# Optimization experiments

Measured on AMD Instinct MI355X. Metric: run time of the kernel, lower is better.

## Reference

```python
import jax, jax.numpy as jnp
import numpy as np

QMIN, QMAX = -128.0, 127.0  # 8-bit signed activation range


def fq_act(x, s):
    """Fake-quantize activations: clip(round(x/s))*s with straight-through estimator."""
    y = jnp.clip(jnp.round(x / s), QMIN, QMAX) * s
    return x + jax.lax.stop_gradient(y - x)


def fq_weight(w):
    """Per-tensor max-abs symmetric (narrow-range) 8-bit weight fake-quant with STE."""
    s = jnp.max(jnp.abs(w)) / 127.0
    y = jnp.clip(jnp.round(w / s), -127.0, 127.0) * s
    return w + jax.lax.stop_gradient(y - w)


def conv1x1(x, w, b):
    # x: [b,c,h,w], w: [o,c] -> [b,o,h,w]
    return jnp.einsum('bchw,oc->bohw', x, w) + b[None, :, None, None]


def setup_inputs() -> dict:
    key = jax.random.key(0)
    ks = jax.random.split(key, 6)
    B, C, HC, H, W = 8, 64, 32, 64, 64
    x = jax.random.normal(ks[0], (B, C, H, W), dtype=jnp.float32)
    wq = jax.random.normal(ks[1], (HC, C), dtype=jnp.float32) * 0.05
    wk = jax.random.normal(ks[2], (HC, C), dtype=jnp.float32) * 0.05
    wv = jax.random.normal(ks[3], (HC, C), dtype=jnp.float32) * 0.05
    wp = jax.random.normal(ks[4], (C, HC), dtype=jnp.float32) * 0.05
    return {
        'x': x,
        'wq': wq, 'bq': jnp.zeros((HC,), jnp.float32),
        'wk': wk, 'bk': jnp.zeros((HC,), jnp.float32),
        'wv': wv, 'bv': jnp.zeros((HC,), jnp.float32),
        'wp': wp, 'bp': jnp.zeros((C,), jnp.float32),
        's_in': jnp.ones((1,), jnp.float32) * 0.0625,
        's_out': jnp.ones((1,), jnp.float32) * 0.0625,
    }


def reference(x, wq, bq, wk, bk, wv, bv, wp, bp, s_in, s_out):
    b, c, h, w = x.shape
    hc = wq.shape[0]
    n = h * w
    xq = fq_act(x, s_in)                              # quant_inp(x)
    q = conv1x1(xq, fq_weight(wq), bq).reshape(b, hc, n).transpose(0, 2, 1)  # [b,n,hc]
    k = conv1x1(xq, fq_weight(wk), bk).reshape(b, hc, n)                     # [b,hc,n]
    v = conv1x1(xq, fq_weight(wv), bv).reshape(b, hc, n).transpose(0, 2, 1)  # [b,n,hc]
    z = jax.nn.softmax(jnp.einsum('bqc,bck->bqk', q, k), axis=-1)            # [b,n,n]
    z = jnp.einsum('bqk,bkc->bqc', z, v).transpose(0, 2, 1).reshape(b, hc, h, w)
    z = fq_act(z, s_in)                               # quant_inp(z) (shared module/scale)
    out = xq + conv1x1(z, fq_weight(wp), bp)
    return fq_act(out, s_out)                         # self.act QuantIdentity
```

## Files before the change

### kernel.cpp

```cpp
#include <hip/hip_runtime.h>
#include <hip/hip_bf16.h>
#include <cstdint>
#include <cstddef>

#define NB 8
#define NC 64
#define NHC 32
#define NN 4096
#define LOG2E 1.44269504088896340736f

typedef short v8s __attribute__((ext_vector_type(8)));
typedef float v4f __attribute__((ext_vector_type(4)));
typedef unsigned int v4u __attribute__((ext_vector_type(4)));

__device__ __forceinline__ unsigned short f2b(float f) {
    unsigned int u = __builtin_bit_cast(unsigned int, f);
    u += 0x7fffu + ((u >> 16) & 1u);
    return (unsigned short)(u >> 16);
}
__device__ __forceinline__ float b2f(unsigned short s) {
    unsigned int u = ((unsigned int)s) << 16;
    return __builtin_bit_cast(float, u);
}
__device__ __forceinline__ unsigned int pack2_bf16(float a, float b) {
    unsigned int ua = __builtin_bit_cast(unsigned int, a);
    ua += 0x7fffu + ((ua >> 16) & 1u);
    unsigned int ub = __builtin_bit_cast(unsigned int, b);
    ub += 0x7fffu + ((ub >> 16) & 1u);
    return (ua >> 16) | (ub & 0xffff0000u);
}
__device__ __forceinline__ unsigned int trunc2_bf16(float a, float b) {
    return __builtin_amdgcn_perm(__builtin_bit_cast(unsigned int, b),
                                 __builtin_bit_cast(unsigned int, a), 0x07060302u);
}
__device__ __forceinline__ float wave_max(float v) {
    #pragma unroll
    for (int off = 1; off < 64; off <<= 1) v = fmaxf(v, __shfl_xor(v, off));
    return v;
}

__global__ __launch_bounds__(256) void k_qkv(
    const float* __restrict__ x,
    const float* __restrict__ wq, const float* __restrict__ wk, const float* __restrict__ wv,
    const float* __restrict__ bq, const float* __restrict__ bk, const float* __restrict__ bv,
    const float* __restrict__ s_in,
    unsigned short* __restrict__ xqb, unsigned short* __restrict__ qb,
    unsigned short* __restrict__ kb, unsigned short* __restrict__ vb)
{
    int blk = blockIdx.x;
    int b   = blk & 7;
    int seg = blk >> 3;
    int p0  = seg * 64;
    int tid = threadIdx.x;
    int wave = tid >> 6;
    int lane = tid & 63;

    __shared__ __align__(16) unsigned short xt[64][72];
    __shared__ __align__(16) unsigned short wlds[6144];
    __shared__ float red[3][4];

    float4 q0 = *(const float4*)(wq + tid * 8), q1 = *(const float4*)(wq + tid * 8 + 4);
    float4 k0 = *(const float4*)(wk + tid * 8), k1 = *(const float4*)(wk + tid * 8 + 4);
    float4 v0 = *(const float4*)(wv + tid * 8), v1 = *(const float4*)(wv + tid * 8 + 4);
    float mq = fmaxf(fmaxf(fmaxf(fabsf(q0.x), fabsf(q0.y)), fmaxf(fabsf(q0.z), fabsf(q0.w))),
                     fmaxf(fmaxf(fabsf(q1.x), fabsf(q1.y)), fmaxf(fabsf(q1.z), fabsf(q1.w))));
    float mk = fmaxf(fmaxf(fmaxf(fabsf(k0.x), fabsf(k0.y)), fmaxf(fabsf(k0.z), fabsf(k0.w))),
                     fmaxf(fmaxf(fabsf(k1.x), fabsf(k1.y)), fmaxf(fabsf(k1.z), fabsf(k1.w))));
    float mv = fmaxf(fmaxf(fmaxf(fabsf(v0.x), fabsf(v0.y)), fmaxf(fabsf(v0.z), fabsf(v0.w))),
                     fmaxf(fmaxf(fabsf(v1.x), fabsf(v1.y)), fmaxf(fabsf(v1.z), fabsf(v1.w))));
    mq = wave_max(mq); mk = wave_max(mk); mv = wave_max(mv);
    if (lane == 0) { red[0][wave] = mq; red[1][wave] = mk; red[2][wave] = mv; }
    __syncthreads();
    float sq = fmaxf(fmaxf(red[0][0], red[0][1]), fmaxf(red[0][2], red[0][3])) / 127.0f;
    float sk = fmaxf(fmaxf(red[1][0], red[1][1]), fmaxf(red[1][2], red[1][3])) / 127.0f;
    float sw = fmaxf(fmaxf(red[2][0], red[2][1]), fmaxf(red[2][2], red[2][3])) / 127.0f;
    {
        float eq[8] = {q0.x, q0.y, q0.z, q0.w, q1.x, q1.y, q1.z, q1.w};
        float ek[8] = {k0.x, k0.y, k0.z, k0.w, k1.x, k1.y, k1.z, k1.w};
        float ev[8] = {v0.x, v0.y, v0.z, v0.w, v1.x, v1.y, v1.z, v1.w};
        #pragma unroll
        for (int j = 0; j < 8; ++j) {
            wlds[0 * 2048 + tid * 8 + j] = f2b(fminf(fmaxf(rintf(eq[j] / sq), -127.f), 127.f) * sq);
            wlds[1 * 2048 + tid * 8 + j] = f2b(fminf(fmaxf(rintf(ek[j] / sk), -127.f), 127.f) * sk);
            wlds[2 * 2048 + tid * 8 + j] = f2b(fminf(fmaxf(rintf(ev[j] / sw), -127.f), 127.f) * sw);
        }
    }

    float sv = s_in[0];
    float sinv = 1.0f / sv;
    int jj = tid & 15;
    int c0 = tid >> 4;
    #pragma unroll
    for (int it = 0; it < 4; ++it) {
        int c = c0 + it * 16;
        size_t gi = ((size_t)(b * NC + c) << 12) + p0 + jj * 4;
        float4 xv = *(const float4*)(x + gi);
        float r0 = fminf(fmaxf(rintf(xv.x * sinv), -128.f), 127.f) * sv;
        float r1 = fminf(fmaxf(rintf(xv.y * sinv), -128.f), 127.f) * sv;
        float r2 = fminf(fmaxf(rintf(xv.z * sinv), -128.f), 127.f) * sv;
        float r3 = fminf(fmaxf(rintf(xv.w * sinv), -128.f), 127.f) * sv;
        *(uint2*)(xqb + gi) = make_uint2(pack2_bf16(r0, r1), pack2_bf16(r2, r3));
        xt[jj * 4 + 0][c] = f2b(r0);
        xt[jj * 4 + 1][c] = f2b(r1);
        xt[jj * 4 + 2][c] = f2b(r2);
        xt[jj * 4 + 3][c] = f2b(r3);
    }
    __syncthreads();

    int quad = lane >> 4;
    int l15  = lane & 15;

    v8s bf0 = *(const v8s*)(&xt[wave * 16 + l15][0  + quad * 8]);
    v8s bf1 = *(const v8s*)(&xt[wave * 16 + l15][32 + quad * 8]);

    int pos = p0 + wave * 16 + l15;
    size_t posg = (size_t)b * NN + pos;
    int g_v  = wave >> 1;
    int hi_v = wave & 1;
    int qs   = l15 >> 2;
    int rr   = l15 & 3;
    int jv   = hi_v * 4 + rr;
    size_t fb = (size_t)b * NN * NHC + (size_t)seg * 2048;
    const v4f zc = {0.f, 0.f, 0.f, 0.f};

    #pragma unroll
    for (int rb = 0; rb < 6; ++rb) {
        v8s a0 = *(const v8s*)(wlds + (rb * 16 + l15) * 64 + 0  + quad * 8);
        v8s a1 = *(const v8s*)(wlds + (rb * 16 + l15) * 64 + 32 + quad * 8);
        v4f t   = __builtin_amdgcn_mfma_f32_16x16x32_bf16(a0, bf0, zc, 0, 0, 0);
        v4f acc = __builtin_amdgcn_mfma_f32_16x16x32_bf16(a1, bf1, t, 0, 0, 0);

        int R0 = rb * 16 + quad * 4;
        float vals[4];
        #pragma unroll
        for (int r = 0; r < 4; ++r) {
            int R = R0 + r;
            float bias = (R < 32) ? bq[R] : (R < 64) ? bk[R - 32] : bv[R - 64];
            float vv = acc[r] + bias;
            if (R < 32) vv *= LOG2E;
            vals[r] = vv;
        }
        if (R0 < 32) {
            *(unsigned int*)(qb + posg * NHC + R0)     = pack2_bf16(vals[0], vals[1]);
            *(unsigned int*)(qb + posg * NHC + R0 + 2) = pack2_bf16(vals[2], vals[3]);
        } else if (R0 < 64) {
            int chb = R0 - 32;
            size_t sidx = fb + (size_t)wave * 512 + ((chb >> 3) * 16 + l15) * 8 + (chb & 7);
            *(uint2*)(kb + sidx) = make_uint2(pack2_bf16(vals[0], vals[1]),
                                              pack2_bf16(vals[2], vals[3]));
        } else {
            int h = rb - 4;
            #pragma unroll
            for (int r = 0; r < 4; ++r) {
                int lp = quad * 4 + r;
                size_t sidx = fb + (size_t)(2 * h + g_v) * 512 + (qs * 16 + lp) * 8 + jv;
                vb[sidx] = f2b(vals[r]);
            }
        }
    }
}

__global__ __launch_bounds__(256, 2) void k_attn(
    const unsigned short* __restrict__ qb, const unsigned short* __restrict__ kb,
    const unsigned short* __restrict__ vb, const unsigned short* __restrict__ xqb,
    const float* __restrict__ wp, const float* __restrict__ bp,
    const float* __restrict__ s_in, const float* __restrict__ s_out,
    float* __restrict__ out)
{
    int blk  = blockIdx.x;
    int b    = blk & 7;
    int qt   = blk >> 3;
    int qbase = qt * 64;
    int tid  = threadIdx.x;
    int wave = tid >> 6;
    int lane = tid & 63;
    int quad = lane >> 4;
    int l15  = lane & 15;

    __shared__ __align__(16) float zbuf[4][64][36];
    __shared__ float lbuf[4][64];
    __shared__ __align__(16) unsigned short wpq[2048];
    __shared__ float redw[4];

    {
        float4 a0 = *(const float4*)(wp + tid * 8), a1 = *(const float4*)(wp + tid * 8 + 4);
        float mx = fmaxf(fmaxf(fmaxf(fabsf(a0.x), fabsf(a0.y)), fmaxf(fabsf(a0.z), fabsf(a0.w))),
                         fmaxf(fmaxf(fabsf(a1.x), fabsf(a1.y)), fmaxf(fabsf(a1.z), fabsf(a1.w))));
        mx = wave_max(mx);
        if (lane == 0) redw[wave] = mx;
        __syncthreads();
        float scale = fmaxf(fmaxf(redw[0], redw[1]), fmaxf(redw[2], redw[3])) / 127.0f;
        float e[8] = {a0.x, a0.y, a0.z, a0.w, a1.x, a1.y, a1.z, a1.w};
        #pragma unroll
        for (int j = 0; j < 8; ++j) {
            float r = fminf(fmaxf(rintf(e[j] / scale), -127.f), 127.f);
            wpq[tid * 8 + j] = f2b(r * scale);
        }
    }

    const unsigned short* qbat = qb + (size_t)b * NN * NHC;
    const unsigned short* kft  = kb + (size_t)b * NN * NHC;
    const unsigned short* vft  = vb + (size_t)b * NN * NHC;

    v8s qf[4];
    #pragma unroll
    for (int s = 0; s < 4; ++s)
        qf[s] = *(const v8s*)(qbat + (qbase + s * 16 + l15) * NHC + quad * 8);

    const v4f zc = {0.f, 0.f, 0.f, 0.f};
    v4f zt[4][2] = {{zc, zc}, {zc, zc}, {zc, zc}, {zc, zc}};
    float psA[4] = {0.f, 0.f, 0.f, 0.f};
    float psB[4] = {0.f, 0.f, 0.f, 0.f};

    int lane8 = lane * 8;
    int t0 = wave * 16;

    const unsigned short* kp = kft + (size_t)t0 * 2048;
    const unsigned short* vp = vft + (size_t)t0 * 2048;
    v8s ck0 = *(const v8s*)(kp + 0 * 512 + lane8);
    v8s ck1 = *(const v8s*)(kp + 1 * 512 + lane8);
    v8s ck2 = *(const v8s*)(kp + 2 * 512 + lane8);
    v8s ck3 = *(const v8s*)(kp + 3 * 512 + lane8);
    v8s cv00 = *(const v8s*)(vp + 0 * 512 + lane8);
    v8s cv01 = *(const v8s*)(vp + 1 * 512 + lane8);
    v8s cv10 = *(const v8s*)(vp + 2 * 512 + lane8);
    v8s cv11 = *(const v8s*)(vp + 3 * 512 + lane8);

    #pragma unroll 1
    for (int i = 0; i < 16; ++i) {
        int ni = wave * 16 + ((i + 1) & 15);
        const unsigned short* kn = kft + (size_t)ni * 2048;
        const unsigned short* vn = vft + (size_t)ni * 2048;
        v8s nk0 = *(const v8s*)(kn + 0 * 512 + lane8);
        v8s nk1 = *(const v8s*)(kn + 1 * 512 + lane8);
        v8s nk2 = *(const v8s*)(kn + 2 * 512 + lane8);
        v8s nk3 = *(const v8s*)(kn + 3 * 512 + lane8);
        v8s nv00 = *(const v8s*)(vn + 0 * 512 + lane8);
        v8s nv01 = *(const v8s*)(vn + 1 * 512 + lane8);
        v8s nv10 = *(const v8s*)(vn + 2 * 512 + lane8);
        v8s nv11 = *(const v8s*)(vn + 3 * 512 + lane8);

        #pragma unroll
        for (int s = 0; s < 4; ++s) {
            v4f sa[4];
            __builtin_amdgcn_s_setprio(1);
            sa[0] = __builtin_amdgcn_mfma_f32_16x16x32_bf16(ck0, qf[s], zc, 0, 0, 0);
            sa[1] = __builtin_amdgcn_mfma_f32_16x16x32_bf16(ck1, qf[s], zc, 0, 0, 0);
            sa[2] = __builtin_amdgcn_mfma_f32_16x16x32_bf16(ck2, qf[s], zc, 0, 0, 0);
            sa[3] = __builtin_amdgcn_mfma_f32_16x16x32_bf16(ck3, qf[s], zc, 0, 0, 0);
            __builtin_amdgcn_s_setprio(0);

            #pragma unroll
            for (int g = 0; g < 2; ++g) {
                float p00 = __builtin_amdgcn_exp2f(sa[2 * g][0]);
                float p01 = __builtin_amdgcn_exp2f(sa[2 * g][1]);
                float p02 = __builtin_amdgcn_exp2f(sa[2 * g][2]);
                float p03 = __builtin_amdgcn_exp2f(sa[2 * g][3]);
                float p10 = __builtin_amdgcn_exp2f(sa[2 * g + 1][0]);
                float p11 = __builtin_amdgcn_exp2f(sa[2 * g + 1][1]);
                float p12 = __builtin_amdgcn_exp2f(sa[2 * g + 1][2]);
                float p13 = __builtin_amdgcn_exp2f(sa[2 * g + 1][3]);
                psA[s] += p00 + p01;
                psB[s] += p02 + p03;
                psA[s] += p10 + p11;
                psB[s] += p12 + p13;
                v4u w;
                w.x = trunc2_bf16(p00, p01);
                w.y = trunc2_bf16(p02, p03);
                w.z = trunc2_bf16(p10, p11);
                w.w = trunc2_bf16(p12, p13);
                v8s pfrag = __builtin_bit_cast(v8s, w);
                __builtin_amdgcn_s_setprio(1);
                if (g == 0) {
                    zt[s][0] = __builtin_amdgcn_mfma_f32_16x16x32_bf16(cv00, pfrag, zt[s][0], 0, 0, 0);
                    zt[s][1] = __builtin_amdgcn_mfma_f32_16x16x32_bf16(cv10, pfrag, zt[s][1], 0, 0, 0);
                } else {
                    zt[s][0] = __builtin_amdgcn_mfma_f32_16x16x32_bf16(cv01, pfrag, zt[s][0], 0, 0, 0);
                    zt[s][1] = __builtin_amdgcn_mfma_f32_16x16x32_bf16(cv11, pfrag, zt[s][1], 0, 0, 0);
                }
                __builtin_amdgcn_s_setprio(0);
            }
        }
        ck0 = nk0; ck1 = nk1; ck2 = nk2; ck3 = nk3;
        cv00 = nv00; cv01 = nv01; cv10 = nv10; cv11 = nv11;
    }

    #pragma unroll
    for (int s = 0; s < 4; ++s) {
        *(v4f*)(&zbuf[wave][s * 16 + l15][     quad * 4]) = zt[s][0];
        *(v4f*)(&zbuf[wave][s * 16 + l15][16 + quad * 4]) = zt[s][1];
        float ps = psA[s] + psB[s];
        ps += __shfl_xor(ps, 16);
        ps += __shfl_xor(ps, 32);
        if (quad == 0) lbuf[wave][s * 16 + l15] = ps;
    }
    __syncthreads();

    int myq = wave * 16 + l15;
    float L = lbuf[0][myq] + lbuf[1][myq] + lbuf[2][myq] + lbuf[3][myq];

    float z[8] = {0.f};
    #pragma unroll
    for (int w = 0; w < 4; ++w) {
        v4f za  = *(const v4f*)(&zbuf[w][myq][quad * 8]);
        v4f zb2 = *(const v4f*)(&zbuf[w][myq][quad * 8 + 4]);
        #pragma unroll
        for (int j = 0; j < 4; ++j) { z[j] += za[j]; z[4 + j] += zb2[j]; }
    }
    float sv = s_in[0], sinv = 1.0f / sv;
    float so = s_out[0], soinv = 1.0f / so;
    float Linv = 1.0f / L;
    unsigned int zp[4];
    #pragma unroll
    for (int jp = 0; jp < 4; ++jp) {
        float a = z[2 * jp]     * Linv;
        float c = z[2 * jp + 1] * Linv;
        a = fminf(fmaxf(rintf(a * sinv), -128.f), 127.f) * sv;
        c = fminf(fmaxf(rintf(c * sinv), -128.f), 127.f) * sv;
        zp[jp] = pack2_bf16(a, c);
    }
    v8s zf = __builtin_bit_cast(v8s, *(uint4*)zp);

    v8s w0f = *(const v8s*)(wpq + ( 0 + l15) * NHC + quad * 8);
    v8s w1f = *(const v8s*)(wpq + (16 + l15) * NHC + quad * 8);
    v8s w2f = *(const v8s*)(wpq + (32 + l15) * NHC + quad * 8);
    v8s w3f = *(const v8s*)(wpq + (48 + l15) * NHC + quad * 8);
    v4f o0 = __builtin_amdgcn_mfma_f32_16x16x32_bf16(w0f, zf, zc, 0, 0, 0);
    v4f o1 = __builtin_amdgcn_mfma_f32_16x16x32_bf16(w1f, zf, zc, 0, 0, 0);
    v4f o2 = __builtin_amdgcn_mfma_f32_16x16x32_bf16(w2f, zf, zc, 0, 0, 0);
    v4f o3 = __builtin_amdgcn_mfma_f32_16x16x32_bf16(w3f, zf, zc, 0, 0, 0);

    int pos = qbase + wave * 16 + l15;
    #pragma unroll
    for (int ot = 0; ot < 4; ++ot) {
        v4f ov = (ot == 0) ? o0 : (ot == 1) ? o1 : (ot == 2) ? o2 : o3;
        #pragma unroll
        for (int r = 0; r < 4; ++r) {
            int oc = ot * 16 + quad * 4 + r;
            size_t idx = (size_t)(b * NC + oc) * NN + pos;
            float val = ov[r] + bp[oc] + b2f(xqb[idx]);
            float f = fminf(fmaxf(rintf(val * soinv), -128.f), 127.f);
            out[idx] = f * so;
        }
    }
}

extern "C" void kernel_launch(void* const* d_in, const int* in_sizes, int n_in,
                              void* d_out, int out_size, void* d_ws, size_t ws_size,
                              hipStream_t stream) {
    const float* x     = (const float*)d_in[0];
    const float* wq    = (const float*)d_in[1];
    const float* bq    = (const float*)d_in[2];
    const float* wk    = (const float*)d_in[3];
    const float* bk    = (const float*)d_in[4];
    const float* wv    = (const float*)d_in[5];
    const float* bv    = (const float*)d_in[6];
    const float* wp    = (const float*)d_in[7];
    const float* bp    = (const float*)d_in[8];
    const float* s_in  = (const float*)d_in[9];
    const float* s_out = (const float*)d_in[10];
    float* out = (float*)d_out;

    char* ws = (char*)d_ws;
    size_t off = 0;
    auto carve = [&](size_t bytes) {
        void* p = ws + off;
        off = (off + bytes + 255) & ~(size_t)255;
        return p;
    };
    unsigned short* xqb = (unsigned short*)carve((size_t)NB * NC * NN * 2);
    unsigned short* qbf = (unsigned short*)carve((size_t)NB * NN * NHC * 2);
    unsigned short* kbf = (unsigned short*)carve((size_t)NB * NN * NHC * 2);
    unsigned short* vbf = (unsigned short*)carve((size_t)NB * NHC * NN * 2);

    hipLaunchKernelGGL(k_qkv, dim3(512), dim3(256), 0, stream,
                       x, wq, wk, wv, bq, bk, bv, s_in, xqb, qbf, kbf, vbf);
    hipLaunchKernelGGL(k_attn, dim3(512), dim3(256), 0, stream,
                       qbf, kbf, vbf, xqb, wp, bp, s_in, s_out, out);
}
```

Baseline: 113.4 us.

## Hoist weight fake-quant into a separate kernel and halve QKV tile size

```diff
diff --git a/kernel.cpp b/kernel.cpp
--- a/kernel.cpp
+++ b/kernel.cpp
@@ -38,10 +38,52 @@
     for (int off = 1; off < 64; off <<= 1) v = fmaxf(v, __shfl_xor(v, off));
     return v;
 }
-
-__global__ __launch_bounds__(256) void k_qkv(
-    const float* __restrict__ x,
-    const float* __restrict__ wq, const float* __restrict__ wk, const float* __restrict__ wv,
+__device__ __forceinline__ float fmax8(float4 a, float4 b) {
+    return fmaxf(fmaxf(fmaxf(fabsf(a.x), fabsf(a.y)), fmaxf(fabsf(a.z), fabsf(a.w))),
+                 fmaxf(fmaxf(fabsf(b.x), fabsf(b.y)), fmaxf(fabsf(b.z), fabsf(b.w))));
+}
+
+__global__ __launch_bounds__(256) void k_wq(
+    const float* __restrict__ wq, const float* __restrict__ wk,
+    const float* __restrict__ wv, const float* __restrict__ wp,
+    unsigned short* __restrict__ wqkvb, unsigned short* __restrict__ wpb)
+{
+    int tid = threadIdx.x;
+    int wave = tid >> 6, lane = tid & 63;
+    __shared__ float red[4][4];
+
+    float4 q0 = *(const float4*)(wq + tid * 8), q1 = *(const float4*)(wq + tid * 8 + 4);
+    float4 k0 = *(const float4*)(wk + tid * 8), k1 = *(const float4*)(wk + tid * 8 + 4);
+    float4 v0 = *(const float4*)(wv + tid * 8), v1 = *(const float4*)(wv + tid * 8 + 4);
+    float4 p0 = *(const float4*)(wp + tid * 8), p1 = *(const float4*)(wp + tid * 8 + 4);
+    float mq = wave_max(fmax8(q0, q1));
+    float mk = wave_max(fmax8(k0, k1));
+    float mv = wave_max(fmax8(v0, v1));
+    float mp = wave_max(fmax8(p0, p1));
+    if (lane == 0) { red[0][wave] = mq; red[1][wave] = mk; red[2][wave] = mv; red[3][wave] = mp; }
+    __syncthreads();
+    float sq = fmaxf(fmaxf(red[0][0], red[0][1]), fmaxf(red[0][2], red[0][3])) / 127.0f;
+    float sk = fmaxf(fmaxf(red[1][0], red[1][1]), fmaxf(red[1][2], red[1][3])) / 127.0f;
+    float sw = fmaxf(fmaxf(red[2][0], red[2][1]), fmaxf(red[2][2], red[2][3])) / 127.0f;
+    float sp = fmaxf(fmaxf(red[3][0], red[3][1]), fmaxf(red[3][2], red[3][3])) / 127.0f;
+
+    unsigned short* oq = wqkvb + (size_t)blockIdx.x * 6144;
+    unsigned short* op = wpb   + (size_t)blockIdx.x * 2048;
+    float eq[8] = {q0.x, q0.y, q0.z, q0.w, q1.x, q1.y, q1.z, q1.w};
+    float ek[8] = {k0.x, k0.y, k0.z, k0.w, k1.x, k1.y, k1.z, k1.w};
+    float ev[8] = {v0.x, v0.y, v0.z, v0.w, v1.x, v1.y, v1.z, v1.w};
+    float ep[8] = {p0.x, p0.y, p0.z, p0.w, p1.x, p1.y, p1.z, p1.w};
+    #pragma unroll
+    for (int j = 0; j < 8; ++j) {
+        oq[0 * 2048 + tid * 8 + j] = f2b(fminf(fmaxf(rintf(eq[j] / sq), -127.f), 127.f) * sq);
+        oq[1 * 2048 + tid * 8 + j] = f2b(fminf(fmaxf(rintf(ek[j] / sk), -127.f), 127.f) * sk);
+        oq[2 * 2048 + tid * 8 + j] = f2b(fminf(fmaxf(rintf(ev[j] / sw), -127.f), 127.f) * sw);
+        op[tid * 8 + j]            = f2b(fminf(fmaxf(rintf(ep[j] / sp), -127.f), 127.f) * sp);
+    }
+}
+
+__global__ __launch_bounds__(256, 4) void k_qkv(
+    const float* __restrict__ x, const unsigned short* __restrict__ wqkvb,
     const float* __restrict__ bq, const float* __restrict__ bk, const float* __restrict__ bv,
     const float* __restrict__ s_in,
     unsigned short* __restrict__ xqb, unsigned short* __restrict__ qb,
@@ -50,83 +92,69 @@
     int blk = blockIdx.x;
     int b   = blk & 7;
     int seg = blk >> 3;
-    int p0  = seg * 64;
+    int p0  = seg * 32;
     int tid = threadIdx.x;
     int wave = tid >> 6;
     int lane = tid & 63;
 
-    __shared__ __align__(16) unsigned short xt[64][72];
-    __shared__ __align__(16) unsigned short wlds[6144];
-    __shared__ float red[3][4];
-
-    float4 q0 = *(const float4*)(wq + tid * 8), q1 = *(const float4*)(wq + tid * 8 + 4);
-    float4 k0 = *(const float4*)(wk + tid * 8), k1 = *(const float4*)(wk + tid * 8 + 4);
-    float4 v0 = *(const float4*)(wv + tid * 8), v1 = *(const float4*)(wv + tid * 8 + 4);
-    float mq = fmaxf(fmaxf(fmaxf(fabsf(q0.x), fabsf(q0.y)), fmaxf(fabsf(q0.z), fabsf(q0.w))),
-                     fmaxf(fmaxf(fabsf(q1.x), fabsf(q1.y)), fmaxf(fabsf(q1.z), fabsf(q1.w))));
-    float mk = fmaxf(fmaxf(fmaxf(fabsf(k0.x), fabsf(k0.y)), fmaxf(fabsf(k0.z), fabsf(k0.w))),
-                     fmaxf(fmaxf(fabsf(k1.x), fabsf(k1.y)), fmaxf(fabsf(k1.z), fabsf(k1.w))));
-    float mv = fmaxf(fmaxf(fmaxf(fabsf(v0.x), fabsf(v0.y)), fmaxf(fabsf(v0.z), fabsf(v0.w))),
-                     fmaxf(fmaxf(fabsf(v1.x), fabsf(v1.y)), fmaxf(fabsf(v1.z), fabsf(v1.w))));
-    mq = wave_max(mq); mk = wave_max(mk); mv = wave_max(mv);
-    if (lane == 0) { red[0][wave] = mq; red[1][wave] = mk; red[2][wave] = mv; }
-    __syncthreads();
-    float sq = fmaxf(fmaxf(red[0][0], red[0][1]), fmaxf(red[0][2], red[0][3])) / 127.0f;
-    float sk = fmaxf(fmaxf(red[1][0], red[1][1]), fmaxf(red[1][2], red[1][3])) / 127.0f;
-    float sw = fmaxf(fmaxf(red[2][0], red[2][1]), fmaxf(red[2][2], red[2][3])) / 127.0f;
-    {
-        float eq[8] = {q0.x, q0.y, q0.z, q0.w, q1.x, q1.y, q1.z, q1.w};
-        float ek[8] = {k0.x, k0.y, k0.z, k0.w, k1.x, k1.y, k1.z, k1.w};
-        float ev[8] = {v0.x, v0.y, v0.z, v0.w, v1.x, v1.y, v1.z, v1.w};
-        #pragma unroll
-        for (int j = 0; j < 8; ++j) {
-            wlds[0 * 2048 + tid * 8 + j] = f2b(fminf(fmaxf(rintf(eq[j] / sq), -127.f), 127.f) * sq);
-            wlds[1 * 2048 + tid * 8 + j] = f2b(fminf(fmaxf(rintf(ek[j] / sk), -127.f), 127.f) * sk);
-            wlds[2 * 2048 + tid * 8 + j] = f2b(fminf(fmaxf(rintf(ev[j] / sw), -127.f), 127.f) * sw);
-        }
-    }
+    __shared__ __align__(16) unsigned short xt[32][72];
+    const unsigned short* wl = wqkvb + (size_t)b * 6144;
 
     float sv = s_in[0];
     float sinv = 1.0f / sv;
-    int jj = tid & 15;
-    int c0 = tid >> 4;
-    #pragma unroll
-    for (int it = 0; it < 4; ++it) {
-        int c = c0 + it * 16;
-        size_t gi = ((size_t)(b * NC + c) << 12) + p0 + jj * 4;
-        float4 xv = *(const float4*)(x + gi);
-        float r0 = fminf(fmaxf(rintf(xv.x * sinv), -128.f), 127.f) * sv;
-        float r1 = fminf(fmaxf(rintf(xv.y * sinv), -128.f), 127.f) * sv;
-        float r2 = fminf(fmaxf(rintf(xv.z * sinv), -128.f), 127.f) * sv;
-        float r3 = fminf(fmaxf(rintf(xv.w * sinv), -128.f), 127.f) * sv;
-        *(uint2*)(xqb + gi) = make_uint2(pack2_bf16(r0, r1), pack2_bf16(r2, r3));
-        xt[jj * 4 + 0][c] = f2b(r0);
-        xt[jj * 4 + 1][c] = f2b(r1);
-        xt[jj * 4 + 2][c] = f2b(r2);
-        xt[jj * 4 + 3][c] = f2b(r3);
+    int jj = tid & 7;
+    int c0 = tid >> 3;
+    size_t gi0 = ((size_t)(b * NC + c0) << 12) + p0 + jj * 4;
+    size_t gi1 = ((size_t)(b * NC + c0 + 32) << 12) + p0 + jj * 4;
+    float4 xv0 = *(const float4*)(x + gi0);
+    float4 xv1 = *(const float4*)(x + gi1);
+    {
+        float r0 = fminf(fmaxf(rintf(xv0.x * sinv), -128.f), 127.f) * sv;
+        float r1 = fminf(fmaxf(rintf(xv0.y * sinv), -128.f), 127.f) * sv;
+        float r2 = fminf(fmaxf(rintf(xv0.z * sinv), -128.f), 127.f) * sv;
+        float r3 = fminf(fmaxf(rintf(xv0.w * sinv), -128.f), 127.f) * sv;
+        *(uint2*)(xqb + gi0) = make_uint2(pack2_bf16(r0, r1), pack2_bf16(r2, r3));
+        xt[jj * 4 + 0][c0] = f2b(r0);
+        xt[jj * 4 + 1][c0] = f2b(r1);
+        xt[jj * 4 + 2][c0] = f2b(r2);
+        xt[jj * 4 + 3][c0] = f2b(r3);
+        float u0 = fminf(fmaxf(rintf(xv1.x * sinv), -128.f), 127.f) * sv;
+        float u1 = fminf(fmaxf(rintf(xv1.y * sinv), -128.f), 127.f) * sv;
+        float u2 = fminf(fmaxf(rintf(xv1.z * sinv), -128.f), 127.f) * sv;
+        float u3 = fminf(fmaxf(rintf(xv1.w * sinv), -128.f), 127.f) * sv;
+        *(uint2*)(xqb + gi1) = make_uint2(pack2_bf16(u0, u1), pack2_bf16(u2, u3));
+        xt[jj * 4 + 0][c0 + 32] = f2b(u0);
+        xt[jj * 4 + 1][c0 + 32] = f2b(u1);
+        xt[jj * 4 + 2][c0 + 32] = f2b(u2);
+        xt[jj * 4 + 3][c0 + 32] = f2b(u3);
     }
     __syncthreads();
 
     int quad = lane >> 4;
     int l15  = lane & 15;
-
-    v8s bf0 = *(const v8s*)(&xt[wave * 16 + l15][0  + quad * 8]);
-    v8s bf1 = *(const v8s*)(&xt[wave * 16 + l15][32 + quad * 8]);
-
-    int pos = p0 + wave * 16 + l15;
+    int ps   = wave >> 1;
+    int rh   = wave & 1;
+
+    v8s bf0 = *(const v8s*)(&xt[ps * 16 + l15][0  + quad * 8]);
+    v8s bf1 = *(const v8s*)(&xt[ps * 16 + l15][32 + quad * 8]);
+
+    int pos = p0 + ps * 16 + l15;
     size_t posg = (size_t)b * NN + pos;
-    int g_v  = wave >> 1;
-    int hi_v = wave & 1;
+    int T   = seg >> 1;
+    int tau = ((seg & 1) << 1) + ps;
+    int g_v  = tau >> 1;
+    int hi_v = tau & 1;
     int qs   = l15 >> 2;
     int rr   = l15 & 3;
     int jv   = hi_v * 4 + rr;
-    size_t fb = (size_t)b * NN * NHC + (size_t)seg * 2048;
+    size_t fb = (size_t)b * NN * NHC + (size_t)T * 2048;
     const v4f zc = {0.f, 0.f, 0.f, 0.f};
 
     #pragma unroll
-    for (int rb = 0; rb < 6; ++rb) {
-        v8s a0 = *(const v8s*)(wlds + (rb * 16 + l15) * 64 + 0  + quad * 8);
-        v8s a1 = *(const v8s*)(wlds + (rb * 16 + l15) * 64 + 32 + quad * 8);
+    for (int j = 0; j < 3; ++j) {
+        int rb = rh * 3 + j;
+        v8s a0 = *(const v8s*)(wl + (rb * 16 + l15) * 64 + 0  + quad * 8);
+        v8s a1 = *(const v8s*)(wl + (rb * 16 + l15) * 64 + 32 + quad * 8);
         v4f t   = __builtin_amdgcn_mfma_f32_16x16x32_bf16(a0, bf0, zc, 0, 0, 0);
         v4f acc = __builtin_amdgcn_mfma_f32_16x16x32_bf16(a1, bf1, t, 0, 0, 0);
 
@@ -145,7 +173,7 @@
             *(unsigned int*)(qb + posg * NHC + R0 + 2) = pack2_bf16(vals[2], vals[3]);
         } else if (R0 < 64) {
             int chb = R0 - 32;
-            size_t sidx = fb + (size_t)wave * 512 + ((chb >> 3) * 16 + l15) * 8 + (chb & 7);
+            size_t sidx = fb + (size_t)tau * 512 + ((chb >> 3) * 16 + l15) * 8 + (chb & 7);
             *(uint2*)(kb + sidx) = make_uint2(pack2_bf16(vals[0], vals[1]),
                                               pack2_bf16(vals[2], vals[3]));
         } else {
@@ -163,7 +191,7 @@
 __global__ __launch_bounds__(256, 2) void k_attn(
     const unsigned short* __restrict__ qb, const unsigned short* __restrict__ kb,
     const unsigned short* __restrict__ vb, const unsigned short* __restrict__ xqb,
-    const float* __restrict__ wp, const float* __restrict__ bp,
+    const unsigned short* __restrict__ wpb, const float* __restrict__ bp,
     const float* __restrict__ s_in, const float* __restrict__ s_out,
     float* __restrict__ out)
 {
@@ -179,24 +207,6 @@
 
     __shared__ __align__(16) float zbuf[4][64][36];
     __shared__ float lbuf[4][64];
-    __shared__ __align__(16) unsigned short wpq[2048];
-    __shared__ float redw[4];
-
-    {
-        float4 a0 = *(const float4*)(wp + tid * 8), a1 = *(const float4*)(wp + tid * 8 + 4);
-        float mx = fmaxf(fmaxf(fmaxf(fabsf(a0.x), fabsf(a0.y)), fmaxf(fabsf(a0.z), fabsf(a0.w))),
-                         fmaxf(fmaxf(fabsf(a1.x), fabsf(a1.y)), fmaxf(fabsf(a1.z), fabsf(a1.w))));
-        mx = wave_max(mx);
-        if (lane == 0) redw[wave] = mx;
-        __syncthreads();
-        float scale = fmaxf(fmaxf(redw[0], redw[1]), fmaxf(redw[2], redw[3])) / 127.0f;
-        float e[8] = {a0.x, a0.y, a0.z, a0.w, a1.x, a1.y, a1.z, a1.w};
-        #pragma unroll
-        for (int j = 0; j < 8; ++j) {
-            float r = fminf(fmaxf(rintf(e[j] / scale), -127.f), 127.f);
-            wpq[tid * 8 + j] = f2b(r * scale);
-        }
-    }
 
     const unsigned short* qbat = qb + (size_t)b * NN * NHC;
     const unsigned short* kft  = kb + (size_t)b * NN * NHC;
@@ -321,10 +331,11 @@
     }
     v8s zf = __builtin_bit_cast(v8s, *(uint4*)zp);
 
-    v8s w0f = *(const v8s*)(wpq + ( 0 + l15) * NHC + quad * 8);
-    v8s w1f = *(const v8s*)(wpq + (16 + l15) * NHC + quad * 8);
-    v8s w2f = *(const v8s*)(wpq + (32 + l15) * NHC + quad * 8);
-    v8s w3f = *(const v8s*)(wpq + (48 + l15) * NHC + quad * 8);
+    const unsigned short* wpl = wpb + (size_t)b * 2048;
+    v8s w0f = *(const v8s*)(wpl + ( 0 + l15) * NHC + quad * 8);
+    v8s w1f = *(const v8s*)(wpl + (16 + l15) * NHC + quad * 8);
+    v8s w2f = *(const v8s*)(wpl + (32 + l15) * NHC + quad * 8);
+    v8s w3f = *(const v8s*)(wpl + (48 + l15) * NHC + quad * 8);
     v4f o0 = __builtin_amdgcn_mfma_f32_16x16x32_bf16(w0f, zf, zc, 0, 0, 0);
     v4f o1 = __builtin_amdgcn_mfma_f32_16x16x32_bf16(w1f, zf, zc, 0, 0, 0);
     v4f o2 = __builtin_amdgcn_mfma_f32_16x16x32_bf16(w2f, zf, zc, 0, 0, 0);
@@ -368,13 +379,17 @@
         off = (off + bytes + 255) & ~(size_t)255;
         return p;
     };
-    unsigned short* xqb = (unsigned short*)carve((size_t)NB * NC * NN * 2);
-    unsigned short* qbf = (unsigned short*)carve((size_t)NB * NN * NHC * 2);
-    unsigned short* kbf = (unsigned short*)carve((size_t)NB * NN * NHC * 2);
-    unsigned short* vbf = (unsigned short*)carve((size_t)NB * NHC * NN * 2);
-
-    hipLaunchKernelGGL(k_qkv, dim3(512), dim3(256), 0, stream,
-                       x, wq, wk, wv, bq, bk, bv, s_in, xqb, qbf, kbf, vbf);
+    unsigned short* xqb   = (unsigned short*)carve((size_t)NB * NC * NN * 2);
+    unsigned short* qbf   = (unsigned short*)carve((size_t)NB * NN * NHC * 2);
+    unsigned short* kbf   = (unsigned short*)carve((size_t)NB * NN * NHC * 2);
+    unsigned short* vbf   = (unsigned short*)carve((size_t)NB * NHC * NN * 2);
+    unsigned short* wqkvb = (unsigned short*)carve((size_t)8 * 6144 * 2);
+    unsigned short* wpb   = (unsigned short*)carve((size_t)8 * 2048 * 2);
+
+    hipLaunchKernelGGL(k_wq, dim3(8), dim3(256), 0, stream,
+                       wq, wk, wv, wp, wqkvb, wpb);
+    hipLaunchKernelGGL(k_qkv, dim3(1024), dim3(256), 0, stream,
+                       x, wqkvb, bq, bk, bv, s_in, xqb, qbf, kbf, vbf);
     hipLaunchKernelGGL(k_attn, dim3(512), dim3(256), 0, stream,
-                       qbf, kbf, vbf, xqb, wp, bp, s_in, s_out, out);
-}
+                       qbf, kbf, vbf, xqb, wpb, bp, s_in, s_out, out);
+}
```

Result: slower. 117.3 us (+3.4%).
